# Kernel optimization log

Measured on AMD Instinct MI355X. Metric: run time of the kernel, lower is better.

The kernel has to match this reference:

```python
import jax, jax.numpy as jnp
import numpy as np

N = 100000   # nodes
E = 800000   # edges
D = 64       # feature dim (input=hidden=output)
EPS = 1e-5   # BatchNorm eps


def setup_inputs() -> dict:
    key = jax.random.key(0)
    ks = jax.random.split(key, 24)
    s = 1.0 / np.sqrt(D)
    inp = {
        "x": jax.random.normal(ks[0], (N, D), jnp.float32),
        "edge_index": jax.random.randint(ks[1], (2, E), 0, N, jnp.int64),
        # GCNConv weights (x @ W + b after normalized aggregation)
        "W1": jax.random.normal(ks[2], (D, D), jnp.float32) * s,
        "b1": jax.random.normal(ks[3], (D,), jnp.float32) * 0.01,
        "W2": jax.random.normal(ks[4], (D, D), jnp.float32) * s,
        "b2": jax.random.normal(ks[5], (D,), jnp.float32) * 0.01,
        "W3": jax.random.normal(ks[6], (D, D), jnp.float32) * s,
        "b3": jax.random.normal(ks[7], (D,), jnp.float32) * 0.01,
        # BatchNorm1d (inference: running stats)
        "bn1_g": jax.random.uniform(ks[8], (D,), jnp.float32, 0.5, 1.5),
        "bn1_b": jax.random.normal(ks[9], (D,), jnp.float32) * 0.1,
        "bn1_m": jax.random.normal(ks[10], (D,), jnp.float32) * 0.1,
        "bn1_v": jax.random.uniform(ks[11], (D,), jnp.float32, 0.5, 1.5),
        "bn2_g": jax.random.uniform(ks[12], (D,), jnp.float32, 0.5, 1.5),
        "bn2_b": jax.random.normal(ks[13], (D,), jnp.float32) * 0.1,
        "bn2_m": jax.random.normal(ks[14], (D,), jnp.float32) * 0.1,
        "bn2_v": jax.random.uniform(ks[15], (D,), jnp.float32, 0.5, 1.5),
        # predictor MLP: Linear -> tanh -> (dropout=id) -> Linear
        "pW1": jax.random.normal(ks[16], (D, D), jnp.float32) * s,
        "pb1": jax.random.normal(ks[17], (D,), jnp.float32) * 0.01,
        "pW2": jax.random.normal(ks[18], (D, D), jnp.float32) * s,
        "pb2": jax.random.normal(ks[19], (D,), jnp.float32) * 0.01,
    }
    return inp


def _gcn_norm(edge_index):
    # add self loops, compute sym-normalized edge coefficients (PyG GCNConv)
    loop = jnp.arange(N, dtype=edge_index.dtype)
    src = jnp.concatenate([edge_index[0], loop])
    dst = jnp.concatenate([edge_index[1], loop])
    deg = jax.ops.segment_sum(jnp.ones(src.shape[0], jnp.float32), dst, num_segments=N)
    dis = jax.lax.rsqrt(deg)  # deg >= 1 due to self loops
    norm = dis[src] * dis[dst]
    return src, dst, norm


def _gcn_layer(x, src, dst, norm, W, b):
    h = x @ W                              # [N, D] small GEMM
    msg = h[src] * norm[:, None]           # [E+N, D] gather (memory bound)
    return jax.ops.segment_sum(msg, dst, num_segments=N) + b  # scatter-add


def _bn(x, g, b, m, v):
    return (x - m) * (g * jax.lax.rsqrt(v + EPS)) + b


def reference(x, edge_index, W1, b1, W2, b2, W3, b3,
              bn1_g, bn1_b, bn1_m, bn1_v, bn2_g, bn2_b, bn2_m, bn2_v,
              pW1, pb1, pW2, pb2):
    src, dst, norm = _gcn_norm(edge_index)
    h = _gcn_layer(x, src, dst, norm, W1, b1)
    h = jax.nn.relu(_bn(h, bn1_g, bn1_b, bn1_m, bn1_v))   # dropout = id (eval)
    h = _gcn_layer(h, src, dst, norm, W2, b2)
    h = jax.nn.relu(_bn(h, bn2_g, bn2_b, bn2_m, bn2_v))
    h = _gcn_layer(h, src, dst, norm, W3, b3)
    out = jnp.tanh(h @ pW1 + pb1) @ pW2 + pb2              # predictor MLP
    return out
```

## Files before the change

### kernel.cpp

```cpp
#include <hip/hip_runtime.h>
#include <hip/hip_fp16.h>

#define N_NODES 100000
#define N_EDGES 800000
#define DIM 64
#define BN_EPS 1e-5f
#define LDX 68
#define EDGE_CAP 1600000

__global__ __launch_bounds__(256) void k_cvt_count(const float* __restrict__ x,
                                                   __half* __restrict__ xh,
                                                   const int* __restrict__ dst,
                                                   int* __restrict__ deg) {
    int idx = blockIdx.x * blockDim.x + threadIdx.x;
    if (idx < 1600000) {
        float4 v = ((const float4*)x)[idx];
        unsigned int u0 = __half_as_ushort(__float2half(v.x));
        unsigned int u1 = __half_as_ushort(__float2half(v.y));
        unsigned int u2 = __half_as_ushort(__float2half(v.z));
        unsigned int u3 = __half_as_ushort(__float2half(v.w));
        ((uint2*)xh)[idx] = make_uint2(u0 | (u1 << 16), u2 | (u3 << 16));
    }
    if (idx < N_EDGES) atomicAdd(&deg[dst[idx]], 1);
}

__global__ __launch_bounds__(256) void k_scan_fuse(const int* __restrict__ deg,
                                                   int* __restrict__ row_off,
                                                   int* __restrict__ cursor,
                                                   float* __restrict__ dinv,
                                                   int* __restrict__ gcount,
                                                   const float* __restrict__ W3,
                                                   const float* __restrict__ b3,
                                                   const float* __restrict__ pW1,
                                                   const float* __restrict__ pb1,
                                                   float* __restrict__ W3p,
                                                   float* __restrict__ b3p) {
    int tid = threadIdx.x;
    if (blockIdx.x == 98) {
        int c = tid & 63;
        int kbase = (tid >> 6) * 16;
        for (int k = kbase; k < kbase + 16; ++k) {
            float acc = 0.f;
#pragma unroll 8
            for (int j = 0; j < 64; ++j)
                acc = fmaf(W3[k * 64 + j], pW1[j * 64 + c], acc);
            W3p[k * 64 + c] = acc;
        }
        if (tid < 64) {
            float acc = pb1[c];
#pragma unroll 8
            for (int j = 0; j < 64; ++j)
                acc = fmaf(b3[j], pW1[j * 64 + c], acc);
            b3p[c] = acc;
        }
        return;
    }
    __shared__ int sdata[256];
    __shared__ int sbase;
    int base = blockIdx.x * 1024 + tid * 4;
    int4 d = make_int4(0, 0, 0, 0);
    int4 v = make_int4(0, 0, 0, 0);
    if (base < N_NODES) {
        d = *(const int4*)(deg + base);
        v.x = (d.x + 7) & ~7;
        v.y = (d.y + 7) & ~7;
        v.z = (d.z + 7) & ~7;
        v.w = (d.w + 7) & ~7;
    }
    int tsum = v.x + v.y + v.z + v.w;
    sdata[tid] = tsum;
    __syncthreads();
    for (int off = 1; off < 256; off <<= 1) {
        int t = (tid >= off) ? sdata[tid - off] : 0;
        __syncthreads();
        sdata[tid] += t;
        __syncthreads();
    }
    if (tid == 255) sbase = atomicAdd(gcount, sdata[255]);
    __syncthreads();
    if (base >= N_NODES) return;
    int excl = sdata[tid] - tsum + sbase;
    int4 o;
    o.x = excl;
    o.y = o.x + v.x;
    o.z = o.y + v.y;
    o.w = o.z + v.z;
    *(int4*)(row_off + base) = o;
    *(int4*)(cursor + base) = o;
    float4 di;
    di.x = rsqrtf((float)(d.x + 1));
    di.y = rsqrtf((float)(d.y + 1));
    di.z = rsqrtf((float)(d.z + 1));
    di.w = rsqrtf((float)(d.w + 1));
    *(float4*)(dinv + base) = di;
}

__global__ __launch_bounds__(256) void k_build(const int* __restrict__ ei,
                                               const float* __restrict__ dinv,
                                               int* __restrict__ cursor,
                                               int2* __restrict__ edges) {
    int part = blockIdx.x & 7;
    int e = (blockIdx.x >> 3) * 256 + threadIdx.x;
    if (e >= N_EDGES) return;
    int d = ei[N_EDGES + e];
    if (d / 12500 != part) return;
    int s = ei[e];
    int pos = atomicAdd(&cursor[d], 1);
    edges[pos] = make_int2(s, __float_as_int(dinv[s] * dinv[d]));
}

__global__ __launch_bounds__(256) void k_aggregate(const __half* __restrict__ xin,
                                                   const int* __restrict__ row_off,
                                                   const int* __restrict__ deg,
                                                   const int2* __restrict__ edges,
                                                   const float* __restrict__ dinv,
                                                   __half* __restrict__ out) {
    int lane16 = threadIdx.x & 15;
    int node = blockIdx.x * 16 + (threadIdx.x >> 4);
    float di = dinv[node];
    int beg = row_off[node];
    int len = deg[node];

    uint2 us = ((const uint2*)(xin + (size_t)node * DIM))[lane16];
    float w0 = di * di;
    float4 acc;
    acc.x = __half2float(__ushort_as_half((unsigned short)(us.x & 0xffff))) * w0;
    acc.y = __half2float(__ushort_as_half((unsigned short)(us.x >> 16))) * w0;
    acc.z = __half2float(__ushort_as_half((unsigned short)(us.y & 0xffff))) * w0;
    acc.w = __half2float(__ushort_as_half((unsigned short)(us.y >> 16))) * w0;

    int lenmax = len;
    lenmax = max(lenmax, __shfl_xor(lenmax, 16, 64));
    lenmax = max(lenmax, __shfl_xor(lenmax, 32, 64));

    int lclamp = (len > 0) ? (len - 1) : 0;
    for (int i = 0; i < lenmax; i += 8) {
#pragma unroll
        for (int u = 0; u < 8; ++u) {
            int j = i + u;
            int jc = j < lclamp ? j : lclamp;
            int2 e = edges[beg + jc];
            int s = ((unsigned)e.x < N_NODES) ? e.x : 0;
            float w = (j < len) ? __int_as_float(e.y) : 0.f;
            uint2 u2 = ((const uint2*)(xin + (size_t)s * DIM))[lane16];
            acc.x = fmaf(w, __half2float(__ushort_as_half((unsigned short)(u2.x & 0xffff))), acc.x);
            acc.y = fmaf(w, __half2float(__ushort_as_half((unsigned short)(u2.x >> 16))), acc.y);
            acc.z = fmaf(w, __half2float(__ushort_as_half((unsigned short)(u2.y & 0xffff))), acc.z);
            acc.w = fmaf(w, __half2float(__ushort_as_half((unsigned short)(u2.y >> 16))), acc.w);
        }
    }

    unsigned int p0 = __half_as_ushort(__float2half(acc.x)) |
                      (__half_as_ushort(__float2half(acc.y)) << 16);
    unsigned int p1 = __half_as_ushort(__float2half(acc.z)) |
                      (__half_as_ushort(__float2half(acc.w)) << 16);
    ((uint2*)(out + (size_t)node * DIM))[lane16] = make_uint2(p0, p1);
}

#define GEMM_STEP(SX, SW)                                                      \
    {                                                                          \
        float4 a0 = *(const float4*)&SX[(r0 + 0) * LDX + k4 * 4];              \
        float4 a1 = *(const float4*)&SX[(r0 + 1) * LDX + k4 * 4];              \
        float4 a2 = *(const float4*)&SX[(r0 + 2) * LDX + k4 * 4];              \
        float4 a3 = *(const float4*)&SX[(r0 + 3) * LDX + k4 * 4];              \
        float4 b0 = *(const float4*)&SW[(k4 * 4 + 0) * 64 + c0];               \
        float4 b1 = *(const float4*)&SW[(k4 * 4 + 1) * 64 + c0];               \
        float4 b2 = *(const float4*)&SW[(k4 * 4 + 2) * 64 + c0];               \
        float4 b3 = *(const float4*)&SW[(k4 * 4 + 3) * 64 + c0];               \
        const float* ap[4] = {&a0.x, &a1.x, &a2.x, &a3.x};                     \
        _Pragma("unroll") for (int i = 0; i < 4; ++i) {                        \
            float x0 = ap[i][0], x1 = ap[i][1], x2 = ap[i][2], x3 = ap[i][3];  \
            acc[i][0] = fmaf(x0, b0.x, acc[i][0]);                             \
            acc[i][1] = fmaf(x0, b0.y, acc[i][1]);                             \
            acc[i][2] = fmaf(x0, b0.z, acc[i][2]);                             \
            acc[i][3] = fmaf(x0, b0.w, acc[i][3]);                             \
            acc[i][0] = fmaf(x1, b1.x, acc[i][0]);                             \
            acc[i][1] = fmaf(x1, b1.y, acc[i][1]);                             \
            acc[i][2] = fmaf(x1, b1.z, acc[i][2]);                             \
            acc[i][3] = fmaf(x1, b1.w, acc[i][3]);                             \
            acc[i][0] = fmaf(x2, b2.x, acc[i][0]);                             \
            acc[i][1] = fmaf(x2, b2.y, acc[i][1]);                             \
            acc[i][2] = fmaf(x2, b2.z, acc[i][2]);                             \
            acc[i][3] = fmaf(x2, b2.w, acc[i][3]);                             \
            acc[i][0] = fmaf(x3, b3.x, acc[i][0]);                             \
            acc[i][1] = fmaf(x3, b3.y, acc[i][1]);                             \
            acc[i][2] = fmaf(x3, b3.z, acc[i][2]);                             \
            acc[i][3] = fmaf(x3, b3.w, acc[i][3]);                             \
        }                                                                      \
    }

#define STAGE_H2F(SRCPTR, SXPTR)                                               \
    {                                                                          \
        int r = tid >> 2;                                                      \
        int q = tid & 3;                                                       \
        int row = row0 + r;                                                    \
        float4* dst = (float4*)(SXPTR + r * LDX);                              \
        if (row < N_NODES) {                                                   \
            const uint2* src = (const uint2*)(SRCPTR + (size_t)row * DIM);     \
            _Pragma("unroll") for (int m = 0; m < 4; ++m) {                    \
                uint2 u = src[q + m * 4];                                      \
                float4 f;                                                      \
                f.x = __half2float(__ushort_as_half((unsigned short)(u.x & 0xffff)));       \
                f.y = __half2float(__ushort_as_half((unsigned short)(u.x >> 16)));          \
                f.z = __half2float(__ushort_as_half((unsigned short)(u.y & 0xffff)));       \
                f.w = __half2float(__ushort_as_half((unsigned short)(u.y >> 16)));          \
                dst[q + m * 4] = f;                                            \
            }                                                                  \
        } else {                                                               \
            float4 z = make_float4(0.f, 0.f, 0.f, 0.f);                        \
            _Pragma("unroll") for (int m = 0; m < 4; ++m) dst[q + m * 4] = z;  \
        }                                                                      \
    }

__global__ __launch_bounds__(256) void k_gemm_bn_h(const __half* __restrict__ xin,
                                                   const float* __restrict__ W,
                                                   const float* __restrict__ bias,
                                                   const float* __restrict__ bng,
                                                   const float* __restrict__ bnb,
                                                   const float* __restrict__ bnm,
                                                   const float* __restrict__ bnv,
                                                   __half* __restrict__ out) {
    __shared__ float sW[4096];
    __shared__ float sX[64 * LDX];
    int tid = threadIdx.x;
    int row0 = blockIdx.x * 64;

    for (int i = tid; i < 1024; i += 256)
        ((float4*)sW)[i] = ((const float4*)W)[i];
    STAGE_H2F(xin, sX)
    __syncthreads();

    int cq = tid & 15, rq = tid >> 4;
    int c0 = cq * 4, r0 = rq * 4;
    float acc[4][4];
#pragma unroll
    for (int i = 0; i < 4; ++i)
#pragma unroll
        for (int j = 0; j < 4; ++j) acc[i][j] = 0.f;

#pragma unroll 4
    for (int k4 = 0; k4 < 16; ++k4) GEMM_STEP(sX, sW)

    float4 bv = *(const float4*)&bias[c0];
    float4 g = *(const float4*)&bng[c0];
    float4 bb = *(const float4*)&bnb[c0];
    float4 m = *(const float4*)&bnm[c0];
    float4 vv = *(const float4*)&bnv[c0];
    float A0 = g.x * rsqrtf(vv.x + BN_EPS);
    float A1 = g.y * rsqrtf(vv.y + BN_EPS);
    float A2 = g.z * rsqrtf(vv.z + BN_EPS);
    float A3 = g.w * rsqrtf(vv.w + BN_EPS);
    float B0 = (bv.x - m.x) * A0 + bb.x;
    float B1 = (bv.y - m.y) * A1 + bb.y;
    float B2 = (bv.z - m.z) * A2 + bb.z;
    float B3 = (bv.w - m.w) * A3 + bb.w;
#pragma unroll
    for (int i = 0; i < 4; ++i) {
        int row = row0 + r0 + i;
        if (row >= N_NODES) break;
        unsigned int u0 = __half_as_ushort(__float2half(fmaxf(0.f, fmaf(acc[i][0], A0, B0))));
        unsigned int u1 = __half_as_ushort(__float2half(fmaxf(0.f, fmaf(acc[i][1], A1, B1))));
        unsigned int u2 = __half_as_ushort(__float2half(fmaxf(0.f, fmaf(acc[i][2], A2, B2))));
        unsigned int u3 = __half_as_ushort(__float2half(fmaxf(0.f, fmaf(acc[i][3], A3, B3))));
        *(uint2*)(out + (size_t)row * DIM + c0) = make_uint2(u0 | (u1 << 16), u2 | (u3 << 16));
    }
}

__global__ __launch_bounds__(256) void k_tail(const __half* __restrict__ xin,
                                              const float* __restrict__ W3p,
                                              const float* __restrict__ b3p,
                                              const float* __restrict__ pW2,
                                              const float* __restrict__ pb2,
                                              float* __restrict__ out) {
    __shared__ float sW1[4096];
    __shared__ float sW2[4096];
    __shared__ float sX[64 * LDX];
    int tid = threadIdx.x;
    int row0 = blockIdx.x * 64;

    for (int i = tid; i < 1024; i += 256) {
        ((float4*)sW1)[i] = ((const float4*)W3p)[i];
        ((float4*)sW2)[i] = ((const float4*)pW2)[i];
    }
    STAGE_H2F(xin, sX)
    __syncthreads();

    int cq = tid & 15, rq = tid >> 4;
    int c0 = cq * 4, r0 = rq * 4;
    float acc[4][4];

#pragma unroll
    for (int i = 0; i < 4; ++i)
#pragma unroll
        for (int j = 0; j < 4; ++j) acc[i][j] = 0.f;
#pragma unroll 4
    for (int k4 = 0; k4 < 16; ++k4) GEMM_STEP(sX, sW1)
    __syncthreads();

    {
        float4 bv = *(const float4*)&b3p[c0];
#pragma unroll
        for (int i = 0; i < 4; ++i) {
            float4 h;
            h.x = tanhf(acc[i][0] + bv.x);
            h.y = tanhf(acc[i][1] + bv.y);
            h.z = tanhf(acc[i][2] + bv.z);
            h.w = tanhf(acc[i][3] + bv.w);
            *(float4*)&sX[(r0 + i) * LDX + c0] = h;
        }
    }
    __syncthreads();

#pragma unroll
    for (int i = 0; i < 4; ++i)
#pragma unroll
        for (int j = 0; j < 4; ++j) acc[i][j] = 0.f;
#pragma unroll 4
    for (int k4 = 0; k4 < 16; ++k4) GEMM_STEP(sX, sW2)

    float4 bv = *(const float4*)&pb2[c0];
#pragma unroll
    for (int i = 0; i < 4; ++i) {
        int row = row0 + r0 + i;
        if (row >= N_NODES) break;
        float4 o;
        o.x = acc[i][0] + bv.x;
        o.y = acc[i][1] + bv.y;
        o.z = acc[i][2] + bv.z;
        o.w = acc[i][3] + bv.w;
        *(float4*)(out + (size_t)row * DIM + c0) = o;
    }
}

extern "C" void kernel_launch(void* const* d_in, const int* in_sizes, int n_in,
                              void* d_out, int out_size, void* d_ws, size_t ws_size,
                              hipStream_t stream) {
    const float* x     = (const float*)d_in[0];
    const int*   ei    = (const int*)d_in[1];
    const float* W1    = (const float*)d_in[2];
    const float* b1    = (const float*)d_in[3];
    const float* W2    = (const float*)d_in[4];
    const float* b2    = (const float*)d_in[5];
    const float* W3    = (const float*)d_in[6];
    const float* b3    = (const float*)d_in[7];
    const float* bn1_g = (const float*)d_in[8];
    const float* bn1_b = (const float*)d_in[9];
    const float* bn1_m = (const float*)d_in[10];
    const float* bn1_v = (const float*)d_in[11];
    const float* bn2_g = (const float*)d_in[12];
    const float* bn2_b = (const float*)d_in[13];
    const float* bn2_m = (const float*)d_in[14];
    const float* bn2_v = (const float*)d_in[15];
    const float* pW1   = (const float*)d_in[16];
    const float* pb1   = (const float*)d_in[17];
    const float* pW2   = (const float*)d_in[18];
    const float* pb2   = (const float*)d_in[19];
    float* out = (float*)d_out;

    char* ws = (char*)d_ws;
    int*    deg     = (int*)ws;                      ws += 100352 * 4;
    int*    gcount  = (int*)ws;                      ws += 4 * 4;
    int*    row_off = (int*)ws;                      ws += 100352 * 4;
    int*    cursor  = (int*)ws;                      ws += 100352 * 4;
    int2*   edges   = (int2*)ws;                     ws += (size_t)EDGE_CAP * 8;
    float*  dinv    = (float*)ws;                    ws += 100352 * 4;
    float*  W3p     = (float*)ws;                    ws += 4096 * 4;
    float*  b3p     = (float*)ws;                    ws += 64 * 4;
    __half* xh      = (__half*)ws;                   ws += (size_t)N_NODES * DIM * 2;
    __half* hbuf    = (__half*)ws;                   ws += (size_t)N_NODES * DIM * 2;
    __half* abuf    = (__half*)ws;                   ws += (size_t)N_NODES * DIM * 2;

    const int blk = 256;
    int gCvt   = 6250;
    int gBuild = 3125 * 8;
    int gAgg   = N_NODES / 16;
    int gTile  = (N_NODES + 63) / 64;

    hipMemsetAsync(deg, 0, (size_t)(100352 + 4) * 4, stream);
    k_cvt_count<<<gCvt, blk, 0, stream>>>(x, xh, ei + N_EDGES, deg);
    k_scan_fuse<<<99, blk, 0, stream>>>(deg, row_off, cursor, dinv, gcount,
                                        W3, b3, pW1, pb1, W3p, b3p);
    k_build<<<gBuild, blk, 0, stream>>>(ei, dinv, cursor, edges);

    k_aggregate<<<gAgg, blk, 0, stream>>>(xh, row_off, deg, edges, dinv, abuf);
    k_gemm_bn_h<<<gTile, blk, 0, stream>>>(abuf, W1, b1, bn1_g, bn1_b, bn1_m, bn1_v, hbuf);

    k_aggregate<<<gAgg, blk, 0, stream>>>(hbuf, row_off, deg, edges, dinv, abuf);
    k_gemm_bn_h<<<gTile, blk, 0, stream>>>(abuf, W2, b2, bn2_g, bn2_b, bn2_m, bn2_v, hbuf);

    k_aggregate<<<gAgg, blk, 0, stream>>>(hbuf, row_off, deg, edges, dinv, abuf);
    k_tail<<<gTile, blk, 0, stream>>>(abuf, W3p, b3p, pW2, pb2, out);
}
```

Before: 389.5 us.

## Build CSR via atomic-returned ranks and store source-only edges, computing weights on the fly

The degree-count kernel now records each edge's rank within its destination, returned by the atomic add. That lets the CSR build place every edge with a direct scatter instead of eight partitioned passes with a second atomic cursor. The edge list now stores only the source index, halving its size, and the aggregation kernel recomputes the normalization weight as dinv[src]*dinv[dst]. This removes one atomic pass and a large grid of mostly idle blocks, at the cost of an extra dinv gather per edge in each of the three aggregation passes. Edge order within a row becomes nondeterministic.

```diff
diff --git a/kernel.cpp b/kernel.cpp
--- a/kernel.cpp
+++ b/kernel.cpp
@@ -11,7 +11,8 @@
 __global__ __launch_bounds__(256) void k_cvt_count(const float* __restrict__ x,
                                                    __half* __restrict__ xh,
                                                    const int* __restrict__ dst,
-                                                   int* __restrict__ deg) {
+                                                   int* __restrict__ deg,
+                                                   int* __restrict__ rank) {
     int idx = blockIdx.x * blockDim.x + threadIdx.x;
     if (idx < 1600000) {
         float4 v = ((const float4*)x)[idx];
@@ -21,12 +22,11 @@
         unsigned int u3 = __half_as_ushort(__float2half(v.w));
         ((uint2*)xh)[idx] = make_uint2(u0 | (u1 << 16), u2 | (u3 << 16));
     }
-    if (idx < N_EDGES) atomicAdd(&deg[dst[idx]], 1);
+    if (idx < N_EDGES) rank[idx] = atomicAdd(&deg[dst[idx]], 1);
 }
 
 __global__ __launch_bounds__(256) void k_scan_fuse(const int* __restrict__ deg,
                                                    int* __restrict__ row_off,
-                                                   int* __restrict__ cursor,
                                                    float* __restrict__ dinv,
                                                    int* __restrict__ gcount,
                                                    const float* __restrict__ W3,
@@ -86,7 +86,6 @@
     o.z = o.y + v.y;
     o.w = o.z + v.z;
     *(int4*)(row_off + base) = o;
-    *(int4*)(cursor + base) = o;
     float4 di;
     di.x = rsqrtf((float)(d.x + 1));
     di.y = rsqrtf((float)(d.y + 1));
@@ -96,23 +95,24 @@
 }
 
 __global__ __launch_bounds__(256) void k_build(const int* __restrict__ ei,
-                                               const float* __restrict__ dinv,
-                                               int* __restrict__ cursor,
-                                               int2* __restrict__ edges) {
-    int part = blockIdx.x & 7;
-    int e = (blockIdx.x >> 3) * 256 + threadIdx.x;
-    if (e >= N_EDGES) return;
-    int d = ei[N_EDGES + e];
-    if (d / 12500 != part) return;
-    int s = ei[e];
-    int pos = atomicAdd(&cursor[d], 1);
-    edges[pos] = make_int2(s, __float_as_int(dinv[s] * dinv[d]));
+                                               const int* __restrict__ rank,
+                                               const int* __restrict__ row_off,
+                                               int* __restrict__ esrc) {
+    int idx = blockIdx.x * 256 + threadIdx.x;
+    if (idx >= 200000) return;
+    int4 s4 = ((const int4*)ei)[idx];
+    int4 d4 = ((const int4*)(ei + N_EDGES))[idx];
+    int4 r4 = ((const int4*)rank)[idx];
+    esrc[row_off[d4.x] + r4.x] = s4.x;
+    esrc[row_off[d4.y] + r4.y] = s4.y;
+    esrc[row_off[d4.z] + r4.z] = s4.z;
+    esrc[row_off[d4.w] + r4.w] = s4.w;
 }
 
 __global__ __launch_bounds__(256) void k_aggregate(const __half* __restrict__ xin,
                                                    const int* __restrict__ row_off,
                                                    const int* __restrict__ deg,
-                                                   const int2* __restrict__ edges,
+                                                   const int* __restrict__ esrc,
                                                    const float* __restrict__ dinv,
                                                    __half* __restrict__ out) {
     int lane16 = threadIdx.x & 15;
@@ -139,9 +139,9 @@
         for (int u = 0; u < 8; ++u) {
             int j = i + u;
             int jc = j < lclamp ? j : lclamp;
-            int2 e = edges[beg + jc];
-            int s = ((unsigned)e.x < N_NODES) ? e.x : 0;
-            float w = (j < len) ? __int_as_float(e.y) : 0.f;
+            int s = esrc[beg + jc];
+            s = ((unsigned)s < N_NODES) ? s : 0;
+            float w = (j < len) ? dinv[s] * di : 0.f;
             uint2 u2 = ((const uint2*)(xin + (size_t)s * DIM))[lane16];
             acc.x = fmaf(w, __half2float(__ushort_as_half((unsigned short)(u2.x & 0xffff))), acc.x);
             acc.y = fmaf(w, __half2float(__ushort_as_half((unsigned short)(u2.x >> 16))), acc.y);
@@ -361,8 +361,8 @@
     int*    deg     = (int*)ws;                      ws += 100352 * 4;
     int*    gcount  = (int*)ws;                      ws += 4 * 4;
     int*    row_off = (int*)ws;                      ws += 100352 * 4;
-    int*    cursor  = (int*)ws;                      ws += 100352 * 4;
-    int2*   edges   = (int2*)ws;                     ws += (size_t)EDGE_CAP * 8;
+    int*    rank    = (int*)ws;                      ws += (size_t)N_EDGES * 4;
+    int*    esrc    = (int*)ws;                      ws += (size_t)EDGE_CAP * 4;
     float*  dinv    = (float*)ws;                    ws += 100352 * 4;
     float*  W3p     = (float*)ws;                    ws += 4096 * 4;
     float*  b3p     = (float*)ws;                    ws += 64 * 4;
@@ -372,22 +372,22 @@
 
     const int blk = 256;
     int gCvt   = 6250;
-    int gBuild = 3125 * 8;
+    int gBuild = 782;
     int gAgg   = N_NODES / 16;
     int gTile  = (N_NODES + 63) / 64;
 
     hipMemsetAsync(deg, 0, (size_t)(100352 + 4) * 4, stream);
-    k_cvt_count<<<gCvt, blk, 0, stream>>>(x, xh, ei + N_EDGES, deg);
-    k_scan_fuse<<<99, blk, 0, stream>>>(deg, row_off, cursor, dinv, gcount,
+    k_cvt_count<<<gCvt, blk, 0, stream>>>(x, xh, ei + N_EDGES, deg, rank);
+    k_scan_fuse<<<99, blk, 0, stream>>>(deg, row_off, dinv, gcount,
                                         W3, b3, pW1, pb1, W3p, b3p);
-    k_build<<<gBuild, blk, 0, stream>>>(ei, dinv, cursor, edges);
-
-    k_aggregate<<<gAgg, blk, 0, stream>>>(xh, row_off, deg, edges, dinv, abuf);
+    k_build<<<gBuild, blk, 0, stream>>>(ei, rank, row_off, esrc);
+
+    k_aggregate<<<gAgg, blk, 0, stream>>>(xh, row_off, deg, esrc, dinv, abuf);
     k_gemm_bn_h<<<gTile, blk, 0, stream>>>(abuf, W1, b1, bn1_g, bn1_b, bn1_m, bn1_v, hbuf);
 
-    k_aggregate<<<gAgg, blk, 0, stream>>>(hbuf, row_off, deg, edges, dinv, abuf);
+    k_aggregate<<<gAgg, blk, 0, stream>>>(hbuf, row_off, deg, esrc, dinv, abuf);
     k_gemm_bn_h<<<gTile, blk, 0, stream>>>(abuf, W2, b2, bn2_g, bn2_b, bn2_m, bn2_v, hbuf);
 
-    k_aggregate<<<gAgg, blk, 0, stream>>>(hbuf, row_off, deg, edges, dinv, abuf);
+    k_aggregate<<<gAgg, blk, 0, stream>>>(hbuf, row_off, deg, esrc, dinv, abuf);
     k_tail<<<gTile, blk, 0, stream>>>(abuf, W3p, b3p, pW2, pb2, out);
 }
```

After: 380.5 us. -2.3%, faster.
